# Performance work log

Measured on AMD Instinct MI355X. Metric: run time of the kernel, lower is better.

Reference implementation:

```python
import jax, jax.numpy as jnp
import numpy as np

D = 1536; H = 12; DH = 128; B = 1; S_TXT = 512; S_IMG = 1024; S = S_TXT + S_IMG; FF = 4 * D
EPS = 1e-6


def setup_inputs() -> dict:
    key = jax.random.key(0)
    ks = iter(jax.random.split(key, 64))
    def nrm(shape, s=1.0):
        return jax.random.normal(next(ks), shape, jnp.float32) * s
    w = 0.02
    inp = {}
    inp["hidden_states"] = nrm((B, S_IMG, D))
    inp["encoder_hidden_states"] = nrm((B, S_TXT, D))
    inp["temb"] = nrm((B, D))
    ang = jax.random.uniform(next(ks), (B, S, DH // 2), jnp.float32, 0.0, 2.0 * np.pi)
    c, s = jnp.cos(ang), jnp.sin(ang)
    rot = jnp.stack([jnp.stack([c, -s], -1), jnp.stack([s, c], -1)], -2)  # [B,S,DH/2,2,2]
    inp["image_rotary_emb"] = rot.reshape(1, 1, B * S, DH // 2, 2, 2)
    inp["adaln_img_w"] = nrm((D, 6 * D), w); inp["adaln_img_b"] = jnp.zeros((6 * D,), jnp.float32)
    inp["adaln_txt_w"] = nrm((D, 6 * D), w); inp["adaln_txt_b"] = jnp.zeros((6 * D,), jnp.float32)
    inp["qkv_img_w"] = nrm((D, 3 * D), w); inp["qkv_img_b"] = jnp.zeros((3 * D,), jnp.float32)
    inp["qkv_txt_w"] = nrm((D, 3 * D), w); inp["qkv_txt_b"] = jnp.zeros((3 * D,), jnp.float32)
    inp["q_norm_img"] = jnp.ones((DH,), jnp.float32); inp["k_norm_img"] = jnp.ones((DH,), jnp.float32)
    inp["q_norm_txt"] = jnp.ones((DH,), jnp.float32); inp["k_norm_txt"] = jnp.ones((DH,), jnp.float32)
    inp["out_img_w"] = nrm((D, D), w); inp["out_img_b"] = jnp.zeros((D,), jnp.float32)
    inp["out_txt_w"] = nrm((D, D), w); inp["out_txt_b"] = jnp.zeros((D,), jnp.float32)
    inp["mlp_img_w1"] = nrm((D, FF), w); inp["mlp_img_b1"] = jnp.zeros((FF,), jnp.float32)
    inp["mlp_img_w2"] = nrm((FF, D), w); inp["mlp_img_b2"] = jnp.zeros((D,), jnp.float32)
    inp["mlp_txt_w1"] = nrm((D, FF), w); inp["mlp_txt_b1"] = jnp.zeros((FF,), jnp.float32)
    inp["mlp_txt_w2"] = nrm((FF, D), w); inp["mlp_txt_b2"] = jnp.zeros((D,), jnp.float32)
    return inp


def _ln(x):  # LayerNorm, no affine
    m = jnp.mean(x, -1, keepdims=True)
    v = jnp.mean(jnp.square(x - m), -1, keepdims=True)
    return (x - m) * jax.lax.rsqrt(v + EPS)


def _rms(x, w):  # per-head RMSNorm
    return x * jax.lax.rsqrt(jnp.mean(jnp.square(x), -1, keepdims=True) + EPS) * w


def _rope(x, rot):  # x [B,H,S,DH], rot [B,S,DH/2,2,2]
    xp = x.reshape(*x.shape[:-1], DH // 2, 2)
    out = jnp.einsum('bsdij,bhsdj->bhsdi', rot, xp)
    return out.reshape(x.shape)


def _qkv(x, w, b, qn, kn):  # -> q,k,v each [B,H,S,DH]
    bb, ss, _ = x.shape
    qkv = (x @ w + b).reshape(bb, ss, 3, H, DH).transpose(2, 0, 3, 1, 4)
    q, k, v = qkv[0], qkv[1], qkv[2]
    return _rms(q, qn), _rms(k, kn), v


def _block(hidden_states, encoder_hidden_states, temb, rot,
           adaln_img_w, adaln_img_b, adaln_txt_w, adaln_txt_b,
           qkv_img_w, qkv_img_b, qkv_txt_w, qkv_txt_b,
           q_norm_img, k_norm_img, q_norm_txt, k_norm_txt,
           out_img_w, out_img_b, out_txt_w, out_txt_b,
           mlp_img_w1, mlp_img_b1, mlp_img_w2, mlp_img_b2,
           mlp_txt_w1, mlp_txt_b1, mlp_txt_w2, mlp_txt_b2):
    bsz = hidden_states.shape[0]
    s_txt = encoder_hidden_states.shape[1]
    t = jax.nn.silu(temb)
    emb_i = t @ adaln_img_w + adaln_img_b
    emb_t = t @ adaln_txt_w + adaln_txt_b
    sh_i, sc_i, g_i, shm_i, scm_i, gm_i = [e[:, None, :] for e in jnp.split(emb_i, 6, -1)]
    sh_t, sc_t, g_t, shm_t, scm_t, gm_t = [e[:, None, :] for e in jnp.split(emb_t, 6, -1)]

    n_img = _ln(hidden_states) * (1.0 + sc_i) + sh_i
    n_txt = _ln(encoder_hidden_states) * (1.0 + sc_t) + sh_t

    qi, ki, vi = _qkv(n_img, qkv_img_w, qkv_img_b, q_norm_img, k_norm_img)
    qt, kt, vt = _qkv(n_txt, qkv_txt_w, qkv_txt_b, q_norm_txt, k_norm_txt)
    q = jnp.concatenate([qt, qi], axis=2)
    k = jnp.concatenate([kt, ki], axis=2)
    v = jnp.concatenate([vt, vi], axis=2)

    rot = rot.reshape(bsz, q.shape[2], DH // 2, 2, 2)
    q = _rope(q, rot)
    k = _rope(k, rot)

    scale = 1.0 / np.sqrt(DH)
    attn = jax.nn.softmax(jnp.einsum('bhqd,bhkd->bhqk', q, k) * scale, axis=-1)
    o = jnp.einsum('bhqk,bhkd->bhqd', attn, v)          # [B,H,S,DH]
    o = o.transpose(0, 2, 1, 3).reshape(bsz, -1, D)     # [B,S,D]
    a_txt, a_img = o[:, :s_txt], o[:, s_txt:]

    hidden_states = hidden_states + g_i * (a_img @ out_img_w + out_img_b)
    encoder_hidden_states = encoder_hidden_states + g_t * (a_txt @ out_txt_w + out_txt_b)

    n2_img = _ln(hidden_states) * (1.0 + scm_i) + shm_i
    ff_img = jax.nn.gelu(n2_img @ mlp_img_w1 + mlp_img_b1, approximate=True) @ mlp_img_w2 + mlp_img_b2
    hidden_states = hidden_states + gm_i * ff_img

    n2_txt = _ln(encoder_hidden_states) * (1.0 + scm_t) + shm_t
    ff_txt = jax.nn.gelu(n2_txt @ mlp_txt_w1 + mlp_txt_b1, approximate=True) @ mlp_txt_w2 + mlp_txt_b2
    encoder_hidden_states = encoder_hidden_states + gm_t * ff_txt

    return jnp.concatenate([encoder_hidden_states, hidden_states], axis=1)


def reference(hidden_states, encoder_hidden_states, temb, image_rotary_emb,
              adaln_img_w, adaln_img_b, adaln_txt_w, adaln_txt_b,
              qkv_img_w, qkv_img_b, qkv_txt_w, qkv_txt_b,
              q_norm_img, k_norm_img, q_norm_txt, k_norm_txt,
              out_img_w, out_img_b, out_txt_w, out_txt_b,
              mlp_img_w1, mlp_img_b1, mlp_img_w2, mlp_img_b2,
              mlp_txt_w1, mlp_txt_b1, mlp_txt_w2, mlp_txt_b2):
    s_txt = encoder_hidden_states.shape[1]
    out = _block(hidden_states, encoder_hidden_states, temb, image_rotary_emb,
                 adaln_img_w, adaln_img_b, adaln_txt_w, adaln_txt_b,
                 qkv_img_w, qkv_img_b, qkv_txt_w, qkv_txt_b,
                 q_norm_img, k_norm_img, q_norm_txt, k_norm_txt,
                 out_img_w, out_img_b, out_txt_w, out_txt_b,
                 mlp_img_w1, mlp_img_b1, mlp_img_w2, mlp_img_b2,
                 mlp_txt_w1, mlp_txt_b1, mlp_txt_w2, mlp_txt_b2)
    return (out[:, :s_txt], out[:, s_txt:])
```

## Files before the change

kernel.cpp:

```cpp
#include <hip/hip_runtime.h>
#include <hip/hip_bf16.h>

typedef __bf16 bf16_t;
typedef __attribute__((ext_vector_type(4))) float f32x4;
typedef __attribute__((ext_vector_type(8))) bf16_t bf16x8;
typedef __attribute__((ext_vector_type(4))) bf16_t bf16x4;
typedef __attribute__((ext_vector_type(2))) bf16_t bf16x2;

#define D_MODEL 1536
#define NH 12
#define DHD 128
#define S_TXT 512
#define S_TOT 1536
#define FF_DIM 6144
#define KVSPLIT 4
#define HQB 288

__device__ inline bf16x8 ld_frag(const bf16_t* p) {
    bf16x4 a = *(const bf16x4*)p;
    bf16x4 b = *(const bf16x4*)(p + 16);
    bf16x8 r;
    r[0]=a[0]; r[1]=a[1]; r[2]=a[2]; r[3]=a[3];
    r[4]=b[0]; r[5]=b[1]; r[6]=b[2]; r[7]=b[3];
    return r;
}

__device__ inline void gload16(const void* g, void* l) {
    __builtin_amdgcn_global_load_lds((const __attribute__((address_space(1))) unsigned int*)g,
                                     (__attribute__((address_space(3))) unsigned int*)l, 16, 0, 0);
}

__global__ __launch_bounds__(256)
void adaln_p(const float* __restrict__ temb,
             const float* __restrict__ w_img, const float* __restrict__ w_txt,
             float* __restrict__ part) {
    __shared__ float t[192];
    int tid = threadIdx.x;
    int k0 = blockIdx.y * 192;
    if (tid < 192) {
        float x = temb[k0 + tid];
        t[tid] = x / (1.0f + __expf(-x));
    }
    __syncthreads();
    int n_g = blockIdx.x * 256 + tid;
    bool img = n_g < 9216;
    const float* W = img ? w_img : w_txt;
    int n = img ? n_g : n_g - 9216;
    float acc = 0.f;
    for (int kk = 0; kk < 192; kk += 4) {
        acc += t[kk]     * W[(size_t)(k0 + kk) * 9216 + n];
        acc += t[kk + 1] * W[(size_t)(k0 + kk + 1) * 9216 + n];
        acc += t[kk + 2] * W[(size_t)(k0 + kk + 2) * 9216 + n];
        acc += t[kk + 3] * W[(size_t)(k0 + kk + 3) * 9216 + n];
    }
    part[(size_t)blockIdx.y * 18432 + n_g] = acc;
}

__global__ __launch_bounds__(256)
void adaln_r(const float* __restrict__ part,
             const float* __restrict__ b_img, const float* __restrict__ b_txt,
             float* __restrict__ emb_img, float* __restrict__ emb_txt) {
    int n_g = blockIdx.x * 256 + threadIdx.x;
    float a = 0.f;
#pragma unroll
    for (int kc = 0; kc < 8; ++kc) a += part[(size_t)kc * 18432 + n_g];
    if (n_g < 9216) emb_img[n_g] = a + b_img[n_g];
    else            emb_txt[n_g - 9216] = a + b_txt[n_g - 9216];
}

__global__ __launch_bounds__(256)
void ln_mod(const float* __restrict__ src_txt, const float* __restrict__ src_img,
            const float* __restrict__ emb_t, const float* __restrict__ emb_i,
            int sh_c, int sc_c, bf16_t* __restrict__ out) {
    int row = blockIdx.x;
    bool txt = row < S_TXT;
    const float* src = txt ? src_txt + (size_t)row * D_MODEL
                           : src_img + (size_t)(row - S_TXT) * D_MODEL;
    const float* emb = txt ? emb_t : emb_i;
    int tid = threadIdx.x;
    float2 v[3];
    float s = 0.f, sq = 0.f;
#pragma unroll
    for (int i = 0; i < 3; ++i) {
        v[i] = *(const float2*)(src + tid * 2 + 512 * i);
        s  += v[i].x + v[i].y;
        sq += v[i].x * v[i].x + v[i].y * v[i].y;
    }
#pragma unroll
    for (int off = 32; off > 0; off >>= 1) {
        s  += __shfl_down(s, off);
        sq += __shfl_down(sq, off);
    }
    __shared__ float red[8];
    int wave = tid >> 6, lane = tid & 63;
    if (lane == 0) { red[wave] = s; red[4 + wave] = sq; }
    __syncthreads();
    float ts = red[0] + red[1] + red[2] + red[3];
    float tq = red[4] + red[5] + red[6] + red[7];
    float mean = ts * (1.0f / D_MODEL);
    float var  = tq * (1.0f / D_MODEL) - mean * mean;
    float rstd = rsqrtf(var + 1e-6f);
    bf16_t* op = out + (size_t)row * D_MODEL;
#pragma unroll
    for (int i = 0; i < 3; ++i) {
        int c0 = tid * 2 + 512 * i;
        bf16x2 r;
        r[0] = (bf16_t)((v[i].x - mean) * rstd * (1.0f + emb[sc_c * D_MODEL + c0])     + emb[sh_c * D_MODEL + c0]);
        r[1] = (bf16_t)((v[i].y - mean) * rstd * (1.0f + emb[sc_c * D_MODEL + c0 + 1]) + emb[sh_c * D_MODEL + c0 + 1]);
        *(bf16x2*)(op + c0) = r;
    }
}

template <int K, int N>
__global__ __launch_bounds__(256)
void conv_wt(const float* __restrict__ w_t, const float* __restrict__ w_i,
             bf16_t* __restrict__ dst) {
    __shared__ float tile[64][65];
    const float* src = blockIdx.z ? w_i : w_t;
    bf16_t* d = dst + (size_t)blockIdx.z * N * K;
    int bn = blockIdx.x * 64, bk = blockIdx.y * 64;
    int tid = threadIdx.x;
#pragma unroll
    for (int j = 0; j < 16; ++j) {
        int l = tid + 256 * j;
        int k = l >> 6, n = l & 63;
        tile[k][n] = src[(size_t)(bk + k) * N + bn + n];
    }
    __syncthreads();
#pragma unroll
    for (int j = 0; j < 16; ++j) {
        int l = tid + 256 * j;
        int n = l >> 6, k = l & 63;
        d[(size_t)(bn + n) * K + bk + k] = (bf16_t)tile[k][n];
    }
}

template <int EPI, typename OutT>
__global__ __launch_bounds__(256)
void gemm2(const bf16_t* __restrict__ A, int lda,
           const bf16_t* __restrict__ Wt, int wimg_off,
           const float* __restrict__ bias_t, const float* __restrict__ bias_i,
           const float* __restrict__ resid_t, const float* __restrict__ resid_i, int ldr,
           const float* __restrict__ gate_t, const float* __restrict__ gate_i,
           OutT* __restrict__ out, int ldo, int K) {
    __shared__ bf16_t As[2][128 * 64];
    __shared__ bf16_t Bs[2][128 * 64];
    const int tid = threadIdx.x;

    const int nbx = gridDim.x;
    const int nwg = nbx * gridDim.y;
    int lb = blockIdx.y * nbx + blockIdx.x;
    if ((nwg & 7) == 0) lb = (lb & 7) * (nwg >> 3) + (lb >> 3);
    const int bm = (lb / nbx) * 128, bn = (lb % nbx) * 128;

    const bool txt = bm < S_TXT;
    const bf16_t* W = txt ? Wt : Wt + wimg_off;
    const float* bias = txt ? bias_t : bias_i;
    const int wave = tid >> 6, lane = tid & 63;
    const int wr = (wave >> 1) * 64, wc = (wave & 1) * 64;
    const int lr = lane & 15, lg = lane >> 4;

    const int srow = wave * 8 + (lane >> 3);
    const int csrc = ((lane & 7) ^ ((lane >> 3) & 7)) * 8;
    const bf16_t* Ab = A + (size_t)(bm + srow) * lda + csrc;
    const bf16_t* Wb = W + (size_t)(bn + srow) * K + csrc;
    const int ldst = (wave * 8) * 64;

    f32x4 acc[4][4] = {};
    const int nt = K >> 6;

    auto stage = [&](int buf, int t) {
#pragma unroll
        for (int j = 0; j < 4; ++j) {
            gload16(Ab + (size_t)j * 32 * lda + t * 64, &As[buf][ldst + j * 2048]);
            gload16(Wb + (size_t)j * 32 * K   + t * 64, &Bs[buf][ldst + j * 2048]);
        }
    };

    stage(0, 0);
    asm volatile("s_waitcnt vmcnt(0)" ::: "memory");
    __builtin_amdgcn_s_barrier();

    int cur = 0;
    for (int t = 0; t < nt; ++t) {
        if (t + 1 < nt) stage(cur ^ 1, t + 1);
#pragma unroll
        for (int kk = 0; kk < 2; ++kk) {
            bf16x8 af[4], bfm[4];
#pragma unroll
            for (int m = 0; m < 4; ++m) {
                int rr = wr + m * 16 + lr;
                af[m] = *(const bf16x8*)&As[cur][rr * 64 + (((kk * 4 + lg) ^ (lr & 7)) * 8)];
            }
#pragma unroll
            for (int n = 0; n < 4; ++n) {
                int rr = wc + n * 16 + lr;
                bfm[n] = *(const bf16x8*)&Bs[cur][rr * 64 + (((kk * 4 + lg) ^ (lr & 7)) * 8)];
            }
#pragma unroll
            for (int m = 0; m < 4; ++m)
#pragma unroll
                for (int n = 0; n < 4; ++n)
                    acc[m][n] = __builtin_amdgcn_mfma_f32_16x16x32_bf16(af[m], bfm[n], acc[m][n], 0, 0, 0);
        }
        asm volatile("s_waitcnt vmcnt(0)" ::: "memory");
        __builtin_amdgcn_s_barrier();
        cur ^= 1;
    }

    const float* gate  = txt ? gate_t : gate_i;
    const float* resid = txt ? resid_t : resid_i;
    const int rbase = txt ? 0 : S_TXT;
#pragma unroll
    for (int m = 0; m < 4; ++m) {
#pragma unroll
        for (int r = 0; r < 4; ++r) {
            int grow = bm + wr + m * 16 + lg * 4 + r;
#pragma unroll
            for (int n = 0; n < 4; ++n) {
                int gcol = bn + wc + n * 16 + lr;
                float v = acc[m][n][r] + bias[gcol];
                if constexpr (EPI == 1) {
                    float x = v;
                    float th = tanhf(0.7978845608028654f * (x + 0.044715f * x * x * x));
                    v = 0.5f * x * (1.0f + th);
                } else if constexpr (EPI == 2) {
                    v = resid[(size_t)(grow - rbase) * ldr + gcol] + gate[gcol] * v;
                }
                out[(size_t)grow * ldo + gcol] = (OutT)v;
            }
        }
    }
}

__global__ __launch_bounds__(256)
void gemm3(const bf16_t* __restrict__ A, int lda,
           const bf16_t* __restrict__ Wt, int wimg_off,
           const float* __restrict__ bias_t, const float* __restrict__ bias_i,
           const float* __restrict__ resid_t, const float* __restrict__ resid_i, int ldr,
           const float* __restrict__ gate_t, const float* __restrict__ gate_i,
           float* __restrict__ out, int ldo, int K) {
    __shared__ bf16_t As[2][128 * 64];
    __shared__ bf16_t Bs[2][64 * 64];
    const int tid = threadIdx.x;

    const int nbx = gridDim.x;
    const int nwg = nbx * gridDim.y;
    int lb = blockIdx.y * nbx + blockIdx.x;
    if ((nwg & 7) == 0) lb = (lb & 7) * (nwg >> 3) + (lb >> 3);
    const int bm = (lb / nbx) * 128, bn = (lb % nbx) * 64;

    const bool txt = bm < S_TXT;
    const bf16_t* W = txt ? Wt : Wt + wimg_off;
    const float* bias = txt ? bias_t : bias_i;
    const int wave = tid >> 6, lane = tid & 63;
    const int wr = (wave >> 1) * 64, wc = (wave & 1) * 32;
    const int lr = lane & 15, lg = lane >> 4;

    const int srow = wave * 8 + (lane >> 3);
    const int csrc = ((lane & 7) ^ ((lane >> 3) & 7)) * 8;
    const bf16_t* Ab = A + (size_t)(bm + srow) * lda + csrc;
    const bf16_t* Wb = W + (size_t)(bn + srow) * K + csrc;
    const int ldst = (wave * 8) * 64;

    f32x4 acc[4][2] = {};
    const int nt = K >> 6;

    auto stage = [&](int buf, int t) {
#pragma unroll
        for (int j = 0; j < 4; ++j)
            gload16(Ab + (size_t)j * 32 * lda + t * 64, &As[buf][ldst + j * 2048]);
#pragma unroll
        for (int j = 0; j < 2; ++j)
            gload16(Wb + (size_t)j * 32 * K + t * 64, &Bs[buf][ldst + j * 2048]);
    };

    stage(0, 0);
    asm volatile("s_waitcnt vmcnt(0)" ::: "memory");
    __builtin_amdgcn_s_barrier();

    int cur = 0;
    for (int t = 0; t < nt; ++t) {
        if (t + 1 < nt) stage(cur ^ 1, t + 1);
#pragma unroll
        for (int kk = 0; kk < 2; ++kk) {
            bf16x8 af[4], bfm[2];
#pragma unroll
            for (int m = 0; m < 4; ++m) {
                int rr = wr + m * 16 + lr;
                af[m] = *(const bf16x8*)&As[cur][rr * 64 + (((kk * 4 + lg) ^ (lr & 7)) * 8)];
            }
#pragma unroll
            for (int n = 0; n < 2; ++n) {
                int rr = wc + n * 16 + lr;
                bfm[n] = *(const bf16x8*)&Bs[cur][rr * 64 + (((kk * 4 + lg) ^ (lr & 7)) * 8)];
            }
#pragma unroll
            for (int m = 0; m < 4; ++m)
#pragma unroll
                for (int n = 0; n < 2; ++n)
                    acc[m][n] = __builtin_amdgcn_mfma_f32_16x16x32_bf16(af[m], bfm[n], acc[m][n], 0, 0, 0);
        }
        asm volatile("s_waitcnt vmcnt(0)" ::: "memory");
        __builtin_amdgcn_s_barrier();
        cur ^= 1;
    }

    const float* gate  = txt ? gate_t : gate_i;
    const float* resid = txt ? resid_t : resid_i;
    const int rbase = txt ? 0 : S_TXT;
#pragma unroll
    for (int m = 0; m < 4; ++m) {
#pragma unroll
        for (int r = 0; r < 4; ++r) {
            int grow = bm + wr + m * 16 + lg * 4 + r;
#pragma unroll
            for (int n = 0; n < 2; ++n) {
                int gcol = bn + wc + n * 16 + lr;
                float v = acc[m][n][r] + bias[gcol];
                v = resid[(size_t)(grow - rbase) * ldr + gcol] + gate[gcol] * v;
                out[(size_t)grow * ldo + gcol] = v;
            }
        }
    }
}

__global__ __launch_bounds__(128)
void qkv_epi(const bf16_t* __restrict__ qkv, const float* __restrict__ rope,
             const float* __restrict__ qn_i, const float* __restrict__ kn_i,
             const float* __restrict__ qn_t, const float* __restrict__ kn_t,
             bf16_t* __restrict__ qb, bf16_t* __restrict__ kb) {
    int h = blockIdx.x, s = blockIdx.y, dh = threadIdx.x;
    bool txt = s < S_TXT;
    const float* qn = txt ? qn_t : qn_i;
    const float* kn = txt ? kn_t : kn_i;
    const bf16_t* base = qkv + (size_t)s * 4608 + h * DHD + dh;
    float q = (float)base[0];
    float k = (float)base[D_MODEL];
    float qs = q * q, ks = k * k;
#pragma unroll
    for (int off = 32; off > 0; off >>= 1) {
        qs += __shfl_down(qs, off);
        ks += __shfl_down(ks, off);
    }
    __shared__ float red[4];
    if ((threadIdx.x & 63) == 0) {
        red[(threadIdx.x >> 6) * 2]     = qs;
        red[(threadIdx.x >> 6) * 2 + 1] = ks;
    }
    __syncthreads();
    float qr = rsqrtf((red[0] + red[2]) * (1.0f / DHD) + 1e-6f);
    float kr = rsqrtf((red[1] + red[3]) * (1.0f / DHD) + 1e-6f);
    q = q * qr * qn[dh];
    k = k * kr * kn[dh];
    int i = dh & 1, d = dh >> 1;
    const float* rp = rope + ((size_t)s * 64 + d) * 4 + i * 2;
    float r0 = rp[0], r1 = rp[1];
    float qo = __shfl_xor(q, 1), ko = __shfl_xor(k, 1);
    float q0 = i ? qo : q, q1 = i ? q : qo;
    float k0 = i ? ko : k, k1 = i ? k : ko;
    float qq = r0 * q0 + r1 * q1;
    float kk = r0 * k0 + r1 * k1;
    size_t idx = ((size_t)h * S_TOT + s) * DHD + dh;
    qb[idx] = (bf16_t)(qq * 0.08838834764831845f);
    kb[idx] = (bf16_t)kk;
}

__global__ __launch_bounds__(256)
void v_tr(const bf16_t* __restrict__ qkv, bf16_t* __restrict__ vt) {
    __shared__ bf16_t tile[64][130];
    int h = blockIdx.x, sb = blockIdx.y * 64;
    int tid = threadIdx.x;
#pragma unroll
    for (int j = 0; j < 32; ++j) {
        int linear = tid + 256 * j;
        int sl = linear >> 7, dh = linear & 127;
        tile[sl][dh] = qkv[(size_t)(sb + sl) * 4608 + 2 * D_MODEL + h * DHD + dh];
    }
    __syncthreads();
#pragma unroll
    for (int j = 0; j < 32; ++j) {
        int linear = tid + 256 * j;
        int dh = linear >> 6, sl = linear & 63;
        vt[((size_t)h * DHD + dh) * S_TOT + sb + sl] = tile[sl][dh];
    }
}

__global__ __launch_bounds__(256)
void attn_k(const bf16_t* __restrict__ qbuf, const bf16_t* __restrict__ kbuf,
            const bf16_t* __restrict__ vt,
            float* __restrict__ part_o, float* __restrict__ part_ml) {
    __shared__ bf16_t Ks[2][64 * 128];
    __shared__ bf16_t Vs[2][128 * 64];
    __shared__ bf16_t P[4][16 * 64];
    int h = blockIdx.x, qblk = blockIdx.y, z = blockIdx.z;
    int q0 = qblk * 64;
    int tid = threadIdx.x, wave = tid >> 6, lane = tid & 63;
    int lr = lane & 15, lg = lane >> 4;

    const bf16_t* Qp = qbuf + ((size_t)h * S_TOT + q0 + wave * 16 + lr) * DHD;
    bf16x8 qf[4];
#pragma unroll
    for (int kk = 0; kk < 4; ++kk) qf[kk] = *(const bf16x8*)(Qp + (kk * 4 + lg) * 8);

    const int sKr = wave * 4 + (lane >> 4);
    const int cK = lane & 15;
    const bf16_t* Kb = kbuf + ((size_t)h * S_TOT + sKr) * DHD + ((cK ^ (sKr & 7)) * 8);
    const int ldsK = sKr * 128 - (lane >> 4) * 128 + 0;
    const int sVr = wave * 8 + (lane >> 3);
    const int cV = lane & 7;
    const bf16_t* Vb = vt + ((size_t)h * DHD + sVr) * S_TOT + ((cV ^ (sVr & 7)) * 8);
    const int ldsV = (wave * 8) * 64;

    auto stage = [&](int buf, int kb0) {
#pragma unroll
        for (int j = 0; j < 4; ++j) {
            gload16(Kb + (size_t)(kb0 + j * 16) * DHD, &Ks[buf][(wave * 4) * 128 + j * 2048]);
            gload16(Vb + kb0 + (size_t)j * 32 * S_TOT, &Vs[buf][ldsV + j * 2048]);
        }
    };

    f32x4 of[8] = {};
    float m[4] = {-1e30f, -1e30f, -1e30f, -1e30f};
    float l[4] = {};
    const int kv0 = z * (S_TOT / KVSPLIT);
    const int nt = (S_TOT / KVSPLIT) / 64;

    stage(0, kv0);
    asm volatile("s_waitcnt vmcnt(0)" ::: "memory");
    __builtin_amdgcn_s_barrier();

    int cur = 0;
    for (int t = 0; t < nt; ++t) {
        if (t + 1 < nt) stage(cur ^ 1, kv0 + (t + 1) * 64);
        f32x4 sf[4] = {};
        __builtin_amdgcn_s_setprio(1);
#pragma unroll
        for (int n = 0; n < 4; ++n) {
#pragma unroll
            for (int kk = 0; kk < 4; ++kk) {
                bf16x8 kf = *(const bf16x8*)&Ks[cur][(n * 16 + lr) * 128 + (((kk * 4 + lg) ^ (lr & 7)) * 8)];
                sf[n] = __builtin_amdgcn_mfma_f32_16x16x32_bf16(qf[kk], kf, sf[n], 0, 0, 0);
            }
        }
        __builtin_amdgcn_s_setprio(0);
        float bm[4], alpha[4], rs[4];
#pragma unroll
        for (int r = 0; r < 4; ++r)
            bm[r] = fmaxf(fmaxf(sf[0][r], sf[1][r]), fmaxf(sf[2][r], sf[3][r]));
#pragma unroll
        for (int mask = 1; mask < 16; mask <<= 1)
#pragma unroll
            for (int r = 0; r < 4; ++r) bm[r] = fmaxf(bm[r], __shfl_xor(bm[r], mask));
#pragma unroll
        for (int r = 0; r < 4; ++r) {
            float mn = fmaxf(m[r], bm[r]);
            alpha[r] = __expf(m[r] - mn);
            m[r] = mn;
            rs[r] = 0.f;
        }
#pragma unroll
        for (int n = 0; n < 4; ++n)
#pragma unroll
            for (int r = 0; r < 4; ++r) {
                float p = __expf(sf[n][r] - m[r]);
                rs[r] += p;
                int row = lg * 4 + r, col = n * 16 + lr;
                P[wave][row * 64 + ((((col >> 3) ^ (row & 7)) << 3) | (col & 7))] = (bf16_t)p;
            }
#pragma unroll
        for (int mask = 1; mask < 16; mask <<= 1)
#pragma unroll
            for (int r = 0; r < 4; ++r) rs[r] += __shfl_xor(rs[r], mask);
#pragma unroll
        for (int r = 0; r < 4; ++r) l[r] = l[r] * alpha[r] + rs[r];
#pragma unroll
        for (int nf = 0; nf < 8; ++nf)
#pragma unroll
            for (int r = 0; r < 4; ++r) of[nf][r] *= alpha[r];
        __builtin_amdgcn_s_setprio(1);
#pragma unroll
        for (int kk2 = 0; kk2 < 2; ++kk2) {
            bf16x8 pf = *(const bf16x8*)&P[wave][lr * 64 + (((kk2 * 4 + lg) ^ (lr & 7)) * 8)];
#pragma unroll
            for (int nf = 0; nf < 8; ++nf) {
                bf16x8 vf = *(const bf16x8*)&Vs[cur][(nf * 16 + lr) * 64 + (((kk2 * 4 + lg) ^ (lr & 7)) * 8)];
                of[nf] = __builtin_amdgcn_mfma_f32_16x16x32_bf16(pf, vf, of[nf], 0, 0, 0);
            }
        }
        __builtin_amdgcn_s_setprio(0);
        asm volatile("s_waitcnt vmcnt(0)" ::: "memory");
        __builtin_amdgcn_s_barrier();
        cur ^= 1;
    }
    int hqb = h * 24 + qblk;
    float* po = part_o + ((size_t)z * HQB + hqb) * 8192;
    int rb = wave * 16 + lg * 4;
#pragma unroll
    for (int r = 0; r < 4; ++r)
#pragma unroll
        for (int nf = 0; nf < 8; ++nf)
            po[(rb + r) * 128 + nf * 16 + lr] = of[nf][r];
    if (lr == 0) {
#pragma unroll
        for (int r = 0; r < 4; ++r) {
            size_t mi = (((size_t)z * HQB + hqb) * 64 + rb + r) * 2;
            part_ml[mi]     = m[r];
            part_ml[mi + 1] = l[r];
        }
    }
}

__global__ __launch_bounds__(256)
void attn_red(const float* __restrict__ part_o, const float* __restrict__ part_ml,
              bf16_t* __restrict__ o) {
    int hqb = blockIdx.x;
    int h = hqb / 24, q0 = (hqb % 24) * 64;
    __shared__ float wz[KVSPLIT][64];
    __shared__ float invL[64];
    int tid = threadIdx.x;
    if (tid < 64) {
        float mz[KVSPLIT], lz[KVSPLIT];
#pragma unroll
        for (int zz = 0; zz < KVSPLIT; ++zz) {
            size_t mi = (((size_t)zz * HQB + hqb) * 64 + tid) * 2;
            mz[zz] = part_ml[mi];
            lz[zz] = part_ml[mi + 1];
        }
        float M = mz[0];
#pragma unroll
        for (int zz = 1; zz < KVSPLIT; ++zz) M = fmaxf(M, mz[zz]);
        float L = 0.f;
#pragma unroll
        for (int zz = 0; zz < KVSPLIT; ++zz) {
            float w = __expf(mz[zz] - M);
            wz[zz][tid] = w;
            L += w * lz[zz];
        }
        invL[tid] = 1.0f / L;
    }
    __syncthreads();
#pragma unroll
    for (int i = 0; i < 8; ++i) {
        int e4 = tid + 256 * i;
        int row = e4 >> 5, c4 = e4 & 31;
        f32x4 acc = {};
#pragma unroll
        for (int zz = 0; zz < KVSPLIT; ++zz) {
            f32x4 v = *(const f32x4*)&part_o[((size_t)zz * HQB + hqb) * 8192 + row * 128 + c4 * 4];
            float w = wz[zz][row];
            acc[0] += v[0] * w; acc[1] += v[1] * w; acc[2] += v[2] * w; acc[3] += v[3] * w;
        }
        float il = invL[row];
        bf16x4 r;
        r[0] = (bf16_t)(acc[0] * il); r[1] = (bf16_t)(acc[1] * il);
        r[2] = (bf16_t)(acc[2] * il); r[3] = (bf16_t)(acc[3] * il);
        *(bf16x4*)&o[(size_t)(q0 + row) * D_MODEL + h * DHD + c4 * 4] = r;
    }
}

extern "C" void kernel_launch(void* const* d_in, const int* in_sizes, int n_in,
                              void* d_out, int out_size, void* d_ws, size_t ws_size,
                              hipStream_t stream) {
    const float* hidden  = (const float*)d_in[0];
    const float* encoder = (const float*)d_in[1];
    const float* temb    = (const float*)d_in[2];
    const float* rope    = (const float*)d_in[3];
    const float* adaln_img_w = (const float*)d_in[4];
    const float* adaln_img_b = (const float*)d_in[5];
    const float* adaln_txt_w = (const float*)d_in[6];
    const float* adaln_txt_b = (const float*)d_in[7];
    const float* qkv_img_w = (const float*)d_in[8];
    const float* qkv_img_b = (const float*)d_in[9];
    const float* qkv_txt_w = (const float*)d_in[10];
    const float* qkv_txt_b = (const float*)d_in[11];
    const float* qn_img = (const float*)d_in[12];
    const float* kn_img = (const float*)d_in[13];
    const float* qn_txt = (const float*)d_in[14];
    const float* kn_txt = (const float*)d_in[15];
    const float* out_img_w = (const float*)d_in[16];
    const float* out_img_b = (const float*)d_in[17];
    const float* out_txt_w = (const float*)d_in[18];
    const float* out_txt_b = (const float*)d_in[19];
    const float* mlp_img_w1 = (const float*)d_in[20];
    const float* mlp_img_b1 = (const float*)d_in[21];
    const float* mlp_img_w2 = (const float*)d_in[22];
    const float* mlp_img_b2 = (const float*)d_in[23];
    const float* mlp_txt_w1 = (const float*)d_in[24];
    const float* mlp_txt_b1 = (const float*)d_in[25];
    const float* mlp_txt_w2 = (const float*)d_in[26];
    const float* mlp_txt_b2 = (const float*)d_in[27];
    float* dout = (float*)d_out;
    char* wsb = (char*)d_ws;

    float*  emb_i = (float*)(wsb);
    float*  emb_t = (float*)(wsb + 36864);
    bf16_t* wreg  = (bf16_t*)(wsb + 73728);
    float*  part  = (float*)(wsb + 73728);
    float*  part_o = (float*)(wsb + 73728);
    bf16_t* n1    = (bf16_t*)(wsb + 37822464);
    float*  part_ml = (float*)(wsb + 37822464);
    bf16_t* qkvb  = (bf16_t*)(wsb + 42541056);
    bf16_t* obuf  = qkvb;
    bf16_t* ffb   = qkvb + 2359296;
    bf16_t* qb    = (bf16_t*)(wsb + 56696832);
    bf16_t* kb    = (bf16_t*)(wsb + 61415424);
    bf16_t* vt    = (bf16_t*)(wsb + 66134016);

    adaln_p<<<dim3(72, 8), 256, 0, stream>>>(temb, adaln_img_w, adaln_txt_w, part);
    adaln_r<<<72, 256, 0, stream>>>(part, adaln_img_b, adaln_txt_b, emb_i, emb_t);
    ln_mod<<<S_TOT, 256, 0, stream>>>(encoder, hidden, emb_t, emb_i, 0, 1, n1);
    conv_wt<1536, 4608><<<dim3(72, 24, 2), 256, 0, stream>>>(qkv_txt_w, qkv_img_w, wreg);
    gemm2<0, bf16_t><<<dim3(36, 12), 256, 0, stream>>>(
        n1, D_MODEL, wreg, 4608 * 1536, qkv_txt_b, qkv_img_b,
        nullptr, nullptr, 0, nullptr, nullptr, qkvb, 4608, 1536);
    qkv_epi<<<dim3(12, 1536), 128, 0, stream>>>(qkvb, rope, qn_img, kn_img, qn_txt, kn_txt, qb, kb);
    v_tr<<<dim3(12, 24), 256, 0, stream>>>(qkvb, vt);
    attn_k<<<dim3(12, 24, KVSPLIT), 256, 0, stream>>>(qb, kb, vt, part_o, part_ml);
    attn_red<<<HQB, 256, 0, stream>>>(part_o, part_ml, obuf);
    conv_wt<1536, 1536><<<dim3(24, 24, 2), 256, 0, stream>>>(out_txt_w, out_img_w, wreg);
    gemm3<<<dim3(24, 12), 256, 0, stream>>>(
        obuf, D_MODEL, wreg, 1536 * 1536, out_txt_b, out_img_b,
        encoder, hidden, D_MODEL, emb_t + 2 * D_MODEL, emb_i + 2 * D_MODEL,
        dout, D_MODEL, 1536);
    ln_mod<<<S_TOT, 256, 0, stream>>>(dout, dout + (size_t)S_TXT * D_MODEL, emb_t, emb_i, 3, 4, n1);
    conv_wt<1536, 6144><<<dim3(96, 24, 2), 256, 0, stream>>>(mlp_txt_w1, mlp_img_w1, wreg);
    gemm2<1, bf16_t><<<dim3(48, 12), 256, 0, stream>>>(
        n1, D_MODEL, wreg, 6144 * 1536, mlp_txt_b1, mlp_img_b1,
        nullptr, nullptr, 0, nullptr, nullptr, ffb, FF_DIM, 1536);
    conv_wt<6144, 1536><<<dim3(24, 96, 2), 256, 0, stream>>>(mlp_txt_w2, mlp_img_w2, wreg);
    gemm3<<<dim3(24, 12), 256, 0, stream>>>(
        ffb, FF_DIM, wreg, 1536 * 6144, mlp_txt_b2, mlp_img_b2,
        dout, dout + (size_t)S_TXT * D_MODEL, D_MODEL,
        emb_t + 5 * D_MODEL, emb_i + 5 * D_MODEL, dout, D_MODEL, 6144);
    (void)in_sizes; (void)n_in; (void)out_size; (void)ws_size;
}
```

Before: 394.1 us.

## Unify GEMMs into single-buffered 128x64 kernel and vectorize weight conversion

Replaces the double-buffered 128x128 and 128x64 GEMM kernels with one 128x64 single-buffered kernel and doubles the grid for the QKV and MLP-up GEMMs. The smaller LDS footprint and accumulator set are meant to raise occupancy and spread work over more blocks, so other waves can hide memory latency instead of explicit prefetch. The cost is that load and compute no longer overlap within a block, and each A tile is reloaded by twice as many blocks. The weight transpose/convert kernel now uses float4 loads and bf16x4 stores to cut memory instruction count.

```diff
diff --git a/kernel.cpp b/kernel.cpp
--- a/kernel.cpp
+++ b/kernel.cpp
@@ -15,15 +15,6 @@
 #define FF_DIM 6144
 #define KVSPLIT 4
 #define HQB 288
-
-__device__ inline bf16x8 ld_frag(const bf16_t* p) {
-    bf16x4 a = *(const bf16x4*)p;
-    bf16x4 b = *(const bf16x4*)(p + 16);
-    bf16x8 r;
-    r[0]=a[0]; r[1]=a[1]; r[2]=a[2]; r[3]=a[3];
-    r[4]=b[0]; r[5]=b[1]; r[6]=b[2]; r[7]=b[3];
-    return r;
-}
 
 __device__ inline void gload16(const void* g, void* l) {
     __builtin_amdgcn_global_load_lds((const __attribute__((address_space(1))) unsigned int*)g,
@@ -121,43 +112,50 @@
     int bn = blockIdx.x * 64, bk = blockIdx.y * 64;
     int tid = threadIdx.x;
 #pragma unroll
-    for (int j = 0; j < 16; ++j) {
-        int l = tid + 256 * j;
-        int k = l >> 6, n = l & 63;
-        tile[k][n] = src[(size_t)(bk + k) * N + bn + n];
+    for (int j = 0; j < 4; ++j) {
+        int k = (tid >> 4) + 16 * j, c4 = tid & 15;
+        float4 v = *(const float4*)(src + (size_t)(bk + k) * N + bn + c4 * 4);
+        tile[k][c4 * 4 + 0] = v.x;
+        tile[k][c4 * 4 + 1] = v.y;
+        tile[k][c4 * 4 + 2] = v.z;
+        tile[k][c4 * 4 + 3] = v.w;
     }
     __syncthreads();
 #pragma unroll
-    for (int j = 0; j < 16; ++j) {
-        int l = tid + 256 * j;
-        int n = l >> 6, k = l & 63;
-        d[(size_t)(bn + n) * K + bk + k] = (bf16_t)tile[k][n];
+    for (int j = 0; j < 4; ++j) {
+        int n = (tid >> 4) + 16 * j, k4 = tid & 15;
+        bf16x4 o;
+        o[0] = (bf16_t)tile[k4 * 4 + 0][n];
+        o[1] = (bf16_t)tile[k4 * 4 + 1][n];
+        o[2] = (bf16_t)tile[k4 * 4 + 2][n];
+        o[3] = (bf16_t)tile[k4 * 4 + 3][n];
+        *(bf16x4*)(d + (size_t)(bn + n) * K + bk + k4 * 4) = o;
     }
 }
 
 template <int EPI, typename OutT>
 __global__ __launch_bounds__(256)
-void gemm2(const bf16_t* __restrict__ A, int lda,
+void gemmU(const bf16_t* __restrict__ A, int lda,
            const bf16_t* __restrict__ Wt, int wimg_off,
            const float* __restrict__ bias_t, const float* __restrict__ bias_i,
            const float* __restrict__ resid_t, const float* __restrict__ resid_i, int ldr,
            const float* __restrict__ gate_t, const float* __restrict__ gate_i,
            OutT* __restrict__ out, int ldo, int K) {
-    __shared__ bf16_t As[2][128 * 64];
-    __shared__ bf16_t Bs[2][128 * 64];
+    __shared__ bf16_t As[128 * 64];
+    __shared__ bf16_t Bs[64 * 64];
     const int tid = threadIdx.x;
 
     const int nbx = gridDim.x;
     const int nwg = nbx * gridDim.y;
     int lb = blockIdx.y * nbx + blockIdx.x;
     if ((nwg & 7) == 0) lb = (lb & 7) * (nwg >> 3) + (lb >> 3);
-    const int bm = (lb / nbx) * 128, bn = (lb % nbx) * 128;
+    const int bm = (lb / nbx) * 128, bn = (lb % nbx) * 64;
 
     const bool txt = bm < S_TXT;
     const bf16_t* W = txt ? Wt : Wt + wimg_off;
     const float* bias = txt ? bias_t : bias_i;
     const int wave = tid >> 6, lane = tid & 63;
-    const int wr = (wave >> 1) * 64, wc = (wave & 1) * 64;
+    const int wr = (wave >> 1) * 64, wc = (wave & 1) * 32;
     const int lr = lane & 15, lg = lane >> 4;
 
     const int srow = wave * 8 + (lane >> 3);
@@ -166,46 +164,37 @@
     const bf16_t* Wb = W + (size_t)(bn + srow) * K + csrc;
     const int ldst = (wave * 8) * 64;
 
-    f32x4 acc[4][4] = {};
+    f32x4 acc[4][2] = {};
     const int nt = K >> 6;
 
-    auto stage = [&](int buf, int t) {
-#pragma unroll
-        for (int j = 0; j < 4; ++j) {
-            gload16(Ab + (size_t)j * 32 * lda + t * 64, &As[buf][ldst + j * 2048]);
-            gload16(Wb + (size_t)j * 32 * K   + t * 64, &Bs[buf][ldst + j * 2048]);
-        }
-    };
-
-    stage(0, 0);
-    asm volatile("s_waitcnt vmcnt(0)" ::: "memory");
-    __builtin_amdgcn_s_barrier();
-
-    int cur = 0;
     for (int t = 0; t < nt; ++t) {
-        if (t + 1 < nt) stage(cur ^ 1, t + 1);
+#pragma unroll
+        for (int j = 0; j < 4; ++j)
+            gload16(Ab + (size_t)j * 32 * lda + t * 64, &As[ldst + j * 2048]);
+#pragma unroll
+        for (int j = 0; j < 2; ++j)
+            gload16(Wb + (size_t)j * 32 * K + t * 64, &Bs[ldst + j * 2048]);
+        __syncthreads();
 #pragma unroll
         for (int kk = 0; kk < 2; ++kk) {
-            bf16x8 af[4], bfm[4];
+            bf16x8 af[4], bfm[2];
 #pragma unroll
             for (int m = 0; m < 4; ++m) {
                 int rr = wr + m * 16 + lr;
-                af[m] = *(const bf16x8*)&As[cur][rr * 64 + (((kk * 4 + lg) ^ (lr & 7)) * 8)];
+                af[m] = *(const bf16x8*)&As[rr * 64 + (((kk * 4 + lg) ^ (lr & 7)) * 8)];
             }
 #pragma unroll
-            for (int n = 0; n < 4; ++n) {
+            for (int n = 0; n < 2; ++n) {
                 int rr = wc + n * 16 + lr;
-                bfm[n] = *(const bf16x8*)&Bs[cur][rr * 64 + (((kk * 4 + lg) ^ (lr & 7)) * 8)];
+                bfm[n] = *(const bf16x8*)&Bs[rr * 64 + (((kk * 4 + lg) ^ (lr & 7)) * 8)];
             }
 #pragma unroll
             for (int m = 0; m < 4; ++m)
 #pragma unroll
-                for (int n = 0; n < 4; ++n)
+                for (int n = 0; n < 2; ++n)
                     acc[m][n] = __builtin_amdgcn_mfma_f32_16x16x32_bf16(af[m], bfm[n], acc[m][n], 0, 0, 0);
         }
-        asm volatile("s_waitcnt vmcnt(0)" ::: "memory");
-        __builtin_amdgcn_s_barrier();
-        cur ^= 1;
+        __syncthreads();
     }
 
     const float* gate  = txt ? gate_t : gate_i;
@@ -217,7 +206,7 @@
         for (int r = 0; r < 4; ++r) {
             int grow = bm + wr + m * 16 + lg * 4 + r;
 #pragma unroll
-            for (int n = 0; n < 4; ++n) {
+            for (int n = 0; n < 2; ++n) {
                 int gcol = bn + wc + n * 16 + lr;
                 float v = acc[m][n][r] + bias[gcol];
                 if constexpr (EPI == 1) {
@@ -228,98 +217,6 @@
                     v = resid[(size_t)(grow - rbase) * ldr + gcol] + gate[gcol] * v;
                 }
                 out[(size_t)grow * ldo + gcol] = (OutT)v;
-            }
-        }
-    }
-}
-
-__global__ __launch_bounds__(256)
-void gemm3(const bf16_t* __restrict__ A, int lda,
-           const bf16_t* __restrict__ Wt, int wimg_off,
-           const float* __restrict__ bias_t, const float* __restrict__ bias_i,
-           const float* __restrict__ resid_t, const float* __restrict__ resid_i, int ldr,
-           const float* __restrict__ gate_t, const float* __restrict__ gate_i,
-           float* __restrict__ out, int ldo, int K) {
-    __shared__ bf16_t As[2][128 * 64];
-    __shared__ bf16_t Bs[2][64 * 64];
-    const int tid = threadIdx.x;
-
-    const int nbx = gridDim.x;
-    const int nwg = nbx * gridDim.y;
-    int lb = blockIdx.y * nbx + blockIdx.x;
-    if ((nwg & 7) == 0) lb = (lb & 7) * (nwg >> 3) + (lb >> 3);
-    const int bm = (lb / nbx) * 128, bn = (lb % nbx) * 64;
-
-    const bool txt = bm < S_TXT;
-    const bf16_t* W = txt ? Wt : Wt + wimg_off;
-    const float* bias = txt ? bias_t : bias_i;
-    const int wave = tid >> 6, lane = tid & 63;
-    const int wr = (wave >> 1) * 64, wc = (wave & 1) * 32;
-    const int lr = lane & 15, lg = lane >> 4;
-
-    const int srow = wave * 8 + (lane >> 3);
-    const int csrc = ((lane & 7) ^ ((lane >> 3) & 7)) * 8;
-    const bf16_t* Ab = A + (size_t)(bm + srow) * lda + csrc;
-    const bf16_t* Wb = W + (size_t)(bn + srow) * K + csrc;
-    const int ldst = (wave * 8) * 64;
-
-    f32x4 acc[4][2] = {};
-    const int nt = K >> 6;
-
-    auto stage = [&](int buf, int t) {
-#pragma unroll
-        for (int j = 0; j < 4; ++j)
-            gload16(Ab + (size_t)j * 32 * lda + t * 64, &As[buf][ldst + j * 2048]);
-#pragma unroll
-        for (int j = 0; j < 2; ++j)
-            gload16(Wb + (size_t)j * 32 * K + t * 64, &Bs[buf][ldst + j * 2048]);
-    };
-
-    stage(0, 0);
-    asm volatile("s_waitcnt vmcnt(0)" ::: "memory");
-    __builtin_amdgcn_s_barrier();
-
-    int cur = 0;
-    for (int t = 0; t < nt; ++t) {
-        if (t + 1 < nt) stage(cur ^ 1, t + 1);
-#pragma unroll
-        for (int kk = 0; kk < 2; ++kk) {
-            bf16x8 af[4], bfm[2];
-#pragma unroll
-            for (int m = 0; m < 4; ++m) {
-                int rr = wr + m * 16 + lr;
-                af[m] = *(const bf16x8*)&As[cur][rr * 64 + (((kk * 4 + lg) ^ (lr & 7)) * 8)];
-            }
-#pragma unroll
-            for (int n = 0; n < 2; ++n) {
-                int rr = wc + n * 16 + lr;
-                bfm[n] = *(const bf16x8*)&Bs[cur][rr * 64 + (((kk * 4 + lg) ^ (lr & 7)) * 8)];
-            }
-#pragma unroll
-            for (int m = 0; m < 4; ++m)
-#pragma unroll
-                for (int n = 0; n < 2; ++n)
-                    acc[m][n] = __builtin_amdgcn_mfma_f32_16x16x32_bf16(af[m], bfm[n], acc[m][n], 0, 0, 0);
-        }
-        asm volatile("s_waitcnt vmcnt(0)" ::: "memory");
-        __builtin_amdgcn_s_barrier();
-        cur ^= 1;
-    }
-
-    const float* gate  = txt ? gate_t : gate_i;
-    const float* resid = txt ? resid_t : resid_i;
-    const int rbase = txt ? 0 : S_TXT;
-#pragma unroll
-    for (int m = 0; m < 4; ++m) {
-#pragma unroll
-        for (int r = 0; r < 4; ++r) {
-            int grow = bm + wr + m * 16 + lg * 4 + r;
-#pragma unroll
-            for (int n = 0; n < 2; ++n) {
-                int gcol = bn + wc + n * 16 + lr;
-                float v = acc[m][n][r] + bias[gcol];
-                v = resid[(size_t)(grow - rbase) * ldr + gcol] + gate[gcol] * v;
-                out[(size_t)grow * ldo + gcol] = v;
             }
         }
     }
@@ -406,7 +303,6 @@
     const int sKr = wave * 4 + (lane >> 4);
     const int cK = lane & 15;
     const bf16_t* Kb = kbuf + ((size_t)h * S_TOT + sKr) * DHD + ((cK ^ (sKr & 7)) * 8);
-    const int ldsK = sKr * 128 - (lane >> 4) * 128 + 0;
     const int sVr = wave * 8 + (lane >> 3);
     const int cV = lane & 7;
     const bf16_t* Vb = vt + ((size_t)h * DHD + sVr) * S_TOT + ((cV ^ (sVr & 7)) * 8);
@@ -611,7 +507,7 @@
     adaln_r<<<72, 256, 0, stream>>>(part, adaln_img_b, adaln_txt_b, emb_i, emb_t);
     ln_mod<<<S_TOT, 256, 0, stream>>>(encoder, hidden, emb_t, emb_i, 0, 1, n1);
     conv_wt<1536, 4608><<<dim3(72, 24, 2), 256, 0, stream>>>(qkv_txt_w, qkv_img_w, wreg);
-    gemm2<0, bf16_t><<<dim3(36, 12), 256, 0, stream>>>(
+    gemmU<0, bf16_t><<<dim3(72, 12), 256, 0, stream>>>(
         n1, D_MODEL, wreg, 4608 * 1536, qkv_txt_b, qkv_img_b,
         nullptr, nullptr, 0, nullptr, nullptr, qkvb, 4608, 1536);
     qkv_epi<<<dim3(12, 1536), 128, 0, stream>>>(qkvb, rope, qn_img, kn_img, qn_txt, kn_txt, qb, kb);
@@ -619,17 +515,17 @@
     attn_k<<<dim3(12, 24, KVSPLIT), 256, 0, stream>>>(qb, kb, vt, part_o, part_ml);
     attn_red<<<HQB, 256, 0, stream>>>(part_o, part_ml, obuf);
     conv_wt<1536, 1536><<<dim3(24, 24, 2), 256, 0, stream>>>(out_txt_w, out_img_w, wreg);
-    gemm3<<<dim3(24, 12), 256, 0, stream>>>(
+    gemmU<2, float><<<dim3(24, 12), 256, 0, stream>>>(
         obuf, D_MODEL, wreg, 1536 * 1536, out_txt_b, out_img_b,
         encoder, hidden, D_MODEL, emb_t + 2 * D_MODEL, emb_i + 2 * D_MODEL,
         dout, D_MODEL, 1536);
     ln_mod<<<S_TOT, 256, 0, stream>>>(dout, dout + (size_t)S_TXT * D_MODEL, emb_t, emb_i, 3, 4, n1);
     conv_wt<1536, 6144><<<dim3(96, 24, 2), 256, 0, stream>>>(mlp_txt_w1, mlp_img_w1, wreg);
-    gemm2<1, bf16_t><<<dim3(48, 12), 256, 0, stream>>>(
+    gemmU<1, bf16_t><<<dim3(96, 12), 256, 0, stream>>>(
         n1, D_MODEL, wreg, 6144 * 1536, mlp_txt_b1, mlp_img_b1,
         nullptr, nullptr, 0, nullptr, nullptr, ffb, FF_DIM, 1536);
     conv_wt<6144, 1536><<<dim3(24, 96, 2), 256, 0, stream>>>(mlp_txt_w2, mlp_img_w2, wreg);
-    gemm3<<<dim3(24, 12), 256, 0, stream>>>(
+    gemmU<2, float><<<dim3(24, 12), 256, 0, stream>>>(
         ffb, FF_DIM, wreg, 1536 * 6144, mlp_txt_b2, mlp_img_b2,
         dout, dout + (size_t)S_TXT * D_MODEL, D_MODEL,
         emb_t + 5 * D_MODEL, emb_i + 5 * D_MODEL, dout, D_MODEL, 6144);
```

Result: slower. 402.6 us (+2.2%).
